# Performance work log

Measured on AMD Instinct MI355X. Metric: run time of the kernel, lower is better.

Reference implementation:

```python
import jax, jax.numpy as jnp
import numpy as np

B = 65536      # groups per batch
S = 4          # members per group (target_size in source)
D = 256        # embedding_dim
NU = 200000    # num_users
NI = 100000    # num_items
NG = 50000     # num_groups


def setup_inputs() -> dict:
    key = jax.random.key(0)
    ks = jax.random.split(key, 18)
    inp = {
        'group_inputs': jax.random.randint(ks[0], (B,), 0, NG),
        'item_inputs': jax.random.randint(ks[1], (B,), 0, NI),
        'group_members': jax.random.randint(ks[2], (NG, S), 0, NU),
        'user_emb': jax.random.normal(ks[3], (NU, D), jnp.float32) * 0.05,
        'item_emb': jax.random.normal(ks[4], (NI, D), jnp.float32) * 0.05,
        'group_emb': jax.random.normal(ks[5], (NG, D), jnp.float32) * 0.05,
        'att_w1': jax.random.normal(ks[6], (2 * D, 16), jnp.float32) * 0.05,
        'att_b1': jnp.zeros((16,), jnp.float32),
        'att_w2': jax.random.normal(ks[7], (16, 1), jnp.float32) * 0.05,
        'att_b2': jnp.zeros((1,), jnp.float32),
        'cls_w': jax.random.normal(ks[8], (1, 2), jnp.float32),
        'cls_b': jnp.zeros((2,), jnp.float32),
        'pred_w1': jax.random.normal(ks[9], (3 * D, 8), jnp.float32) * 0.05,
        'pred_b1': jnp.zeros((8,), jnp.float32),
        'pred_w2': jax.random.normal(ks[10], (8, 1), jnp.float32) * 0.05,
        'pred_b2': jnp.zeros((1,), jnp.float32),
    }
    return inp


def reference(group_inputs, item_inputs, group_members,
              user_emb, item_emb, group_emb,
              att_w1, att_b1, att_w2, att_b2,
              cls_w, cls_b, pred_w1, pred_b1, pred_w2, pred_b2):
    # gather member ids per group: [B, S]
    mem_idx = group_members[group_inputs]
    members = user_emb[mem_idx]                    # [B, S, D]
    items = item_emb[item_inputs]                  # [B, D]
    items_rep = jnp.broadcast_to(items[:, None, :], members.shape)
    gi = jnp.concatenate([members, items_rep], axis=-1)  # [B, S, 2D]

    # attention MLP: 2D -> 16 -> 1, softmax over members
    h = jax.nn.relu(jnp.einsum('bse,ef->bsf', gi, att_w1) + att_b1)
    logits = (jnp.einsum('bsf,fo->bso', h, att_w2) + att_b2)[..., 0]  # [B, S]
    at_wt = jax.nn.softmax(logits, axis=1)

    max_idx = jnp.argmax(at_wt, axis=1)            # [B]

    # classifier Linear(1,2) applied per attention weight -> [B, S, 2]
    scores = at_wt[..., None] * cls_w[0] + cls_b
    classes = jnp.argmax(scores, axis=-1)          # argmax(softmax)=argmax, [B, S]
    # group-level class = class of the max-weight member
    pred_class = jnp.take_along_axis(classes, max_idx[:, None], axis=1)[:, 0]  # [B]

    # branch: gather argmax member (leader) vs attention-weighted sum
    leader = jnp.take_along_axis(members, max_idx[:, None, None], axis=1)[:, 0, :]
    weighted = jnp.einsum('bs,bsd->bd', at_wt, members)
    g_att = jnp.where((pred_class == 1)[:, None], leader, weighted)

    g = g_att + group_emb[group_inputs]            # [B, D]
    elem = g * items
    new = jnp.concatenate([elem, g, items], axis=-1)   # [B, 3D]
    y = jax.nn.sigmoid(jax.nn.relu(new @ pred_w1 + pred_b1) @ pred_w2 + pred_b2)
    return y, at_wt, pred_class.astype(jnp.float32)
```

## Files before the change

kernel.cpp:

```cpp
#include <hip/hip_runtime.h>

#define NB 65536
#define GPB 16

__device__ __forceinline__ float rs4v(float v0, float v1, float v2, float v3,
                                      bool b0, bool b1) {
    float s, r;
    s = b0 ? v0 : v2; r = __shfl_xor(s, 1); float w0 = (b0 ? v2 : v0) + r;
    s = b0 ? v1 : v3; r = __shfl_xor(s, 1); float w1 = (b0 ? v3 : v1) + r;
    s = b1 ? w0 : w1; r = __shfl_xor(s, 2); float u  = (b1 ? w1 : w0) + r;
    u += __shfl_xor(u, 4);
    u += __shfl_xor(u, 8);
    u += __shfl_xor(u, 16);
    return u;
}

__device__ __forceinline__ float rs8v(float v0, float v1, float v2, float v3,
                                      float v4, float v5, float v6, float v7,
                                      bool b0, bool b1, bool b2) {
    float s, r;
    s = b0 ? v0 : v4; r = __shfl_xor(s, 1); float w0 = (b0 ? v4 : v0) + r;
    s = b0 ? v1 : v5; r = __shfl_xor(s, 1); float w1 = (b0 ? v5 : v1) + r;
    s = b0 ? v2 : v6; r = __shfl_xor(s, 1); float w2 = (b0 ? v6 : v2) + r;
    s = b0 ? v3 : v7; r = __shfl_xor(s, 1); float w3 = (b0 ? v7 : v3) + r;
    s = b1 ? w0 : w2; r = __shfl_xor(s, 2); float x0 = (b1 ? w2 : w0) + r;
    s = b1 ? w1 : w3; r = __shfl_xor(s, 2); float x1 = (b1 ? w3 : w1) + r;
    s = b2 ? x0 : x1; r = __shfl_xor(s, 4); float u = (b2 ? x1 : x0) + r;
    u += __shfl_xor(u, 8);
    u += __shfl_xor(u, 16);
    return u;
}

__global__ __launch_bounds__(256) void agree_kernel(
    const int* __restrict__ group_inputs,
    const int* __restrict__ item_inputs,
    const int* __restrict__ group_members,
    const float* __restrict__ user_emb,
    const float* __restrict__ item_emb,
    const float* __restrict__ group_emb,
    const float* __restrict__ att_w1,
    const float* __restrict__ att_b1,
    const float* __restrict__ att_w2,
    const float* __restrict__ att_b2,
    const float* __restrict__ cls_w,
    const float* __restrict__ cls_b,
    const float* __restrict__ pred_w1,
    const float* __restrict__ pred_b1,
    const float* __restrict__ pred_w2,
    const float* __restrict__ pred_b2,
    float* __restrict__ out)
{
    __shared__ __align__(16) float sBuf[32 * 260];

    const int tid = threadIdx.x;
    const int t = tid & 31;
    const int b0 = blockIdx.x * GPB + ((tid >> 5) << 1);

    const int gA  = group_inputs[b0];
    const int gB  = group_inputs[b0 + 1];
    const int itA = item_inputs[b0];
    const int itB = item_inputs[b0 + 1];
    const int4 mA = ((const int4*)group_members)[gA];
    const int4 mB = ((const int4*)group_members)[gB];

    float mbr[2][4][8];
    {
        const int mi[2][4] = {{mA.x, mA.y, mA.z, mA.w}, {mB.x, mB.y, mB.z, mB.w}};
        #pragma unroll
        for (int gg = 0; gg < 2; ++gg) {
            #pragma unroll
            for (int s = 0; s < 4; ++s) {
                const float4* p = (const float4*)user_emb + (((long)mi[gg][s]) << 6) + (t << 1);
                float4 v0 = p[0], v1 = p[1];
                mbr[gg][s][0] = v0.x; mbr[gg][s][1] = v0.y; mbr[gg][s][2] = v0.z; mbr[gg][s][3] = v0.w;
                mbr[gg][s][4] = v1.x; mbr[gg][s][5] = v1.y; mbr[gg][s][6] = v1.z; mbr[gg][s][7] = v1.w;
            }
        }
    }
    float itv[2][8];
    {
        const int ii[2] = {itA, itB};
        #pragma unroll
        for (int gg = 0; gg < 2; ++gg) {
            const float4* p = (const float4*)item_emb + (((long)ii[gg]) << 6) + (t << 1);
            float4 v0 = p[0], v1 = p[1];
            itv[gg][0] = v0.x; itv[gg][1] = v0.y; itv[gg][2] = v0.z; itv[gg][3] = v0.w;
            itv[gg][4] = v1.x; itv[gg][5] = v1.y; itv[gg][6] = v1.z; itv[gg][7] = v1.w;
        }
    }

    const bool bb0 = (t & 1), bb1 = (t & 2), bb2 = (t & 4);
    const int f4 = ((t & 1) << 1) | ((t >> 1) & 1);
    const int f8 = ((t & 1) << 2) + (t & 2) + ((t >> 2) & 1);
    float ab1v[4], aw2v[4];
    #pragma unroll
    for (int p = 0; p < 4; ++p) {
        ab1v[p] = att_b1[4 * p + f4];
        aw2v[p] = att_w2[4 * p + f4];
    }

    {
        const float4* src = (const float4*)att_w1;
        for (int i = tid; i < 2048; i += 256) {
            float4 v = src[i];
            int r = i >> 2, cb = (i & 3) << 2;
            *(float4*)(sBuf + 260 * (r >> 4) + ((r & 15) << 4) + cb) = v;
        }
    }
    __syncthreads();

    const float* mbase = sBuf + 260 * (t >> 1) + ((t & 1) << 7);
    const float* ibase = mbase + 260 * 16;
    float logit[2][4] = {{0.f, 0.f, 0.f, 0.f}, {0.f, 0.f, 0.f, 0.f}};
    #pragma unroll
    for (int p = 0; p < 4; ++p) {
        float acc[2][4][4], pi[2][4];
        #pragma unroll
        for (int gg = 0; gg < 2; ++gg) {
            #pragma unroll
            for (int f = 0; f < 4; ++f) {
                pi[gg][f] = 0.f;
                #pragma unroll
                for (int s = 0; s < 4; ++s) acc[gg][s][f] = 0.f;
            }
        }
        #pragma unroll
        for (int j = 0; j < 8; ++j) {
            float4 wm = *(const float4*)(mbase + (j << 4) + (p << 2));
            float4 wi = *(const float4*)(ibase + (j << 4) + (p << 2));
            #pragma unroll
            for (int gg = 0; gg < 2; ++gg) {
                #pragma unroll
                for (int s = 0; s < 4; ++s) {
                    float mv = mbr[gg][s][j];
                    acc[gg][s][0] += mv * wm.x; acc[gg][s][1] += mv * wm.y;
                    acc[gg][s][2] += mv * wm.z; acc[gg][s][3] += mv * wm.w;
                }
                float iv = itv[gg][j];
                pi[gg][0] += iv * wi.x; pi[gg][1] += iv * wi.y;
                pi[gg][2] += iv * wi.z; pi[gg][3] += iv * wi.w;
            }
        }
        #pragma unroll
        for (int gg = 0; gg < 2; ++gg) {
            float hb = rs4v(pi[gg][0], pi[gg][1], pi[gg][2], pi[gg][3], bb0, bb1)
                       + ab1v[p];
            #pragma unroll
            for (int s = 0; s < 4; ++s) {
                float h = rs4v(acc[gg][s][0], acc[gg][s][1], acc[gg][s][2], acc[gg][s][3],
                               bb0, bb1) + hb;
                logit[gg][s] += fmaxf(h, 0.f) * aw2v[p];
            }
        }
    }
    #pragma unroll
    for (int gg = 0; gg < 2; ++gg) {
        #pragma unroll
        for (int s = 0; s < 4; ++s) {
            float v = logit[gg][s];
            v += __shfl_xor(v, 1); v += __shfl_xor(v, 2);
            logit[gg][s] = v;
        }
    }

    const float cw0 = cls_w[0], cw1 = cls_w[1], cb0c = cls_b[0], cb1c = cls_b[1];
    float at[2][4]; int bestv[2], pcv[2];
    #pragma unroll
    for (int gg = 0; gg < 2; ++gg) {
        float l0 = logit[gg][0], l1 = logit[gg][1], l2 = logit[gg][2], l3 = logit[gg][3];
        float mx = fmaxf(fmaxf(l0, l1), fmaxf(l2, l3));
        float e0 = __expf(l0 - mx), e1 = __expf(l1 - mx);
        float e2 = __expf(l2 - mx), e3 = __expf(l3 - mx);
        float inv = 1.f / (e0 + e1 + e2 + e3);
        at[gg][0] = e0 * inv; at[gg][1] = e1 * inv;
        at[gg][2] = e2 * inv; at[gg][3] = e3 * inv;
        int best = 0; float bv = at[gg][0];
        if (at[gg][1] > bv) { bv = at[gg][1]; best = 1; }
        if (at[gg][2] > bv) { bv = at[gg][2]; best = 2; }
        if (at[gg][3] > bv) { bv = at[gg][3]; best = 3; }
        bestv[gg] = best;
        pcv[gg] = (bv * cw1 + cb1c) > (bv * cw0 + cb0c) ? 1 : 0;
    }

    if (t == 0) {
        #pragma unroll
        for (int gg = 0; gg < 2; ++gg) {
            const int b = b0 + gg;
            *(float4*)(out + NB + 4 * b) = make_float4(at[gg][0], at[gg][1], at[gg][2], at[gg][3]);
            out[5 * NB + b] = (float)pcv[gg];
        }
    }

    float gvr[2][8];
    {
        const int gi2[2] = {gA, gB};
        #pragma unroll
        for (int gg = 0; gg < 2; ++gg) {
            const float4* p = (const float4*)group_emb + (((long)gi2[gg]) << 6) + (t << 1);
            float4 v0 = p[0], v1 = p[1];
            gvr[gg][0] = v0.x; gvr[gg][1] = v0.y; gvr[gg][2] = v0.z; gvr[gg][3] = v0.w;
            gvr[gg][4] = v1.x; gvr[gg][5] = v1.y; gvr[gg][6] = v1.z; gvr[gg][7] = v1.w;
        }
    }

    __syncthreads();
    {
        const float4* srcp = (const float4*)pred_w1;
        for (int i = tid; i < 1536; i += 256) {
            float4 v = srcp[i];
            int r = i >> 1, cb = (i & 1) << 2;
            *(float4*)(sBuf + 132 * (r >> 4) + ((r & 15) << 3) + cb) = v;
        }
    }

    float gvec[2][8], elv[2][8];
    #pragma unroll
    for (int gg = 0; gg < 2; ++gg) {
        #pragma unroll
        for (int d = 0; d < 8; ++d) {
            float w = at[gg][0] * mbr[gg][0][d] + at[gg][1] * mbr[gg][1][d]
                    + at[gg][2] * mbr[gg][2][d] + at[gg][3] * mbr[gg][3][d];
            float ldr = mbr[gg][0][d];
            ldr = (bestv[gg] == 1) ? mbr[gg][1][d] : ldr;
            ldr = (bestv[gg] == 2) ? mbr[gg][2][d] : ldr;
            ldr = (bestv[gg] == 3) ? mbr[gg][3][d] : ldr;
            float ga = pcv[gg] ? ldr : w;
            float gv = ga + gvr[gg][d];
            gvec[gg][d] = gv;
            elv[gg][d]  = gv * itv[gg][d];
        }
    }
    __syncthreads();

    const float pb1v = pred_b1[f8], pw2v = pred_w2[f8], pb2v = pred_b2[0];
    const float* pbase = sBuf + 132 * (t >> 1) + ((t & 1) << 6);
    float po[2][8] = {{0.f,0.f,0.f,0.f,0.f,0.f,0.f,0.f},
                      {0.f,0.f,0.f,0.f,0.f,0.f,0.f,0.f}};
    #pragma unroll
    for (int j = 0; j < 8; ++j) {
        const float* pA = pbase + (j << 3);
        float4 a0 = *(const float4*)pA,          a1 = *(const float4*)(pA + 4);
        float4 q0 = *(const float4*)(pA + 2112), q1 = *(const float4*)(pA + 2116);
        float4 c0 = *(const float4*)(pA + 4224), c1 = *(const float4*)(pA + 4228);
        #pragma unroll
        for (int gg = 0; gg < 2; ++gg) {
            float e = elv[gg][j], gv = gvec[gg][j], iv = itv[gg][j];
            po[gg][0] += e * a0.x; po[gg][0] += gv * q0.x; po[gg][0] += iv * c0.x;
            po[gg][1] += e * a0.y; po[gg][1] += gv * q0.y; po[gg][1] += iv * c0.y;
            po[gg][2] += e * a0.z; po[gg][2] += gv * q0.z; po[gg][2] += iv * c0.z;
            po[gg][3] += e * a0.w; po[gg][3] += gv * q0.w; po[gg][3] += iv * c0.w;
            po[gg][4] += e * a1.x; po[gg][4] += gv * q1.x; po[gg][4] += iv * c1.x;
            po[gg][5] += e * a1.y; po[gg][5] += gv * q1.y; po[gg][5] += iv * c1.y;
            po[gg][6] += e * a1.z; po[gg][6] += gv * q1.z; po[gg][6] += iv * c1.z;
            po[gg][7] += e * a1.w; po[gg][7] += gv * q1.w; po[gg][7] += iv * c1.w;
        }
    }

    float yv[2];
    #pragma unroll
    for (int gg = 0; gg < 2; ++gg) {
        float poR = rs8v(po[gg][0], po[gg][1], po[gg][2], po[gg][3],
                         po[gg][4], po[gg][5], po[gg][6], po[gg][7],
                         bb0, bb1, bb2);
        float z = fmaxf(poR + pb1v, 0.f) * pw2v;
        z += __shfl_xor(z, 1); z += __shfl_xor(z, 2); z += __shfl_xor(z, 4);
        z += pb2v;
        yv[gg] = 1.f / (1.f + __expf(-z));
    }

    if (t == 0) {
        out[b0]     = yv[0];
        out[b0 + 1] = yv[1];
    }
}

extern "C" void kernel_launch(void* const* d_in, const int* in_sizes, int n_in,
                              void* d_out, int out_size, void* d_ws, size_t ws_size,
                              hipStream_t stream) {
    (void)in_sizes; (void)n_in; (void)out_size; (void)d_ws; (void)ws_size;
    agree_kernel<<<NB / GPB, 256, 0, stream>>>(
        (const int*)d_in[0], (const int*)d_in[1], (const int*)d_in[2],
        (const float*)d_in[3], (const float*)d_in[4], (const float*)d_in[5],
        (const float*)d_in[6], (const float*)d_in[7], (const float*)d_in[8],
        (const float*)d_in[9], (const float*)d_in[10], (const float*)d_in[11],
        (const float*)d_in[12], (const float*)d_in[13], (const float*)d_in[14],
        (const float*)d_in[15], (float*)d_out);
}
```

Baseline: 448.4 us.

## Make kernel persistent with software-pipelined prefetch of next groups' embeddings

Replaces one-shot blocks of 16 groups with 512 blocks that each loop over 8 iterations of 16 groups. Both weight matrices stay resident in separate shared buffers, loaded once per block instead of per 16 groups. The next iteration's indices, member ids and embedding rows are prefetched into a second register set while the current one computes, to hide gather latency. The cost is doubled register state, which may cut occupancy or spill, and far fewer blocks for the GPU's many CUs.

```diff
diff --git a/kernel.cpp b/kernel.cpp
--- a/kernel.cpp
+++ b/kernel.cpp
@@ -1,7 +1,8 @@
 #include <hip/hip_runtime.h>
 
 #define NB 65536
-#define GPB 16
+#define NBLK 512
+#define ITERS 8
 
 __device__ __forceinline__ float rs4v(float v0, float v1, float v2, float v3,
                                       bool b0, bool b1) {
@@ -29,6 +30,225 @@
     u += __shfl_xor(u, 8);
     u += __shfl_xor(u, 16);
     return u;
+}
+
+struct GState {
+    int g0, g1, it0, it1;
+    int4 m0, m1;
+    float mbr[2][4][8];
+    float itv[2][8];
+};
+
+struct Ctx {
+    const int* group_inputs; const int* item_inputs; const int* group_members;
+    const float* user_emb; const float* item_emb; const float* group_emb;
+    float ab1v[4], aw2v[4];
+    float pb1v, pw2v, pb2v, cw0, cw1, cb0c, cb1c;
+    bool bb0, bb1, bb2;
+    int t, lg;
+    float* out;
+};
+
+__device__ __forceinline__ void load_idx(const Ctx& c, GState& st, int b) {
+    st.g0  = c.group_inputs[b];  st.g1  = c.group_inputs[b + 1];
+    st.it0 = c.item_inputs[b];   st.it1 = c.item_inputs[b + 1];
+}
+
+__device__ __forceinline__ void load_mem(const Ctx& c, GState& st) {
+    st.m0 = ((const int4*)c.group_members)[st.g0];
+    st.m1 = ((const int4*)c.group_members)[st.g1];
+}
+
+__device__ __forceinline__ void load_rows(const Ctx& c, GState& st) {
+    const int t = c.t;
+    const int mi[2][4] = {{st.m0.x, st.m0.y, st.m0.z, st.m0.w},
+                          {st.m1.x, st.m1.y, st.m1.z, st.m1.w}};
+    #pragma unroll
+    for (int gg = 0; gg < 2; ++gg) {
+        #pragma unroll
+        for (int s = 0; s < 4; ++s) {
+            const float4* p = (const float4*)c.user_emb + (((long)mi[gg][s]) << 6) + (t << 1);
+            float4 v0 = p[0], v1 = p[1];
+            st.mbr[gg][s][0] = v0.x; st.mbr[gg][s][1] = v0.y;
+            st.mbr[gg][s][2] = v0.z; st.mbr[gg][s][3] = v0.w;
+            st.mbr[gg][s][4] = v1.x; st.mbr[gg][s][5] = v1.y;
+            st.mbr[gg][s][6] = v1.z; st.mbr[gg][s][7] = v1.w;
+        }
+    }
+    const int ii2[2] = {st.it0, st.it1};
+    #pragma unroll
+    for (int gg = 0; gg < 2; ++gg) {
+        const float4* p = (const float4*)c.item_emb + (((long)ii2[gg]) << 6) + (t << 1);
+        float4 v0 = p[0], v1 = p[1];
+        st.itv[gg][0] = v0.x; st.itv[gg][1] = v0.y;
+        st.itv[gg][2] = v0.z; st.itv[gg][3] = v0.w;
+        st.itv[gg][4] = v1.x; st.itv[gg][5] = v1.y;
+        st.itv[gg][6] = v1.z; st.itv[gg][7] = v1.w;
+    }
+}
+
+__device__ __forceinline__ void iter_body(const Ctx& c, GState& cur, GState& nxt,
+                                          int k, int base,
+                                          const float* sA, const float* sP) {
+    const int t = c.t;
+    const int b0 = base + k * 16 + c.lg * 2;
+    const bool more = (k + 1 < ITERS);
+    if (more) load_idx(c, nxt, b0 + 16);
+
+    float gvr[2][8];
+    {
+        const int gi2[2] = {cur.g0, cur.g1};
+        #pragma unroll
+        for (int gg = 0; gg < 2; ++gg) {
+            const float4* p = (const float4*)c.group_emb + (((long)gi2[gg]) << 6) + (t << 1);
+            float4 v0 = p[0], v1 = p[1];
+            gvr[gg][0] = v0.x; gvr[gg][1] = v0.y; gvr[gg][2] = v0.z; gvr[gg][3] = v0.w;
+            gvr[gg][4] = v1.x; gvr[gg][5] = v1.y; gvr[gg][6] = v1.z; gvr[gg][7] = v1.w;
+        }
+    }
+
+    const float* mbase = sA + 260 * (t >> 1) + ((t & 1) << 7);
+    const float* ibase = mbase + 260 * 16;
+    float logit[2][4] = {{0.f, 0.f, 0.f, 0.f}, {0.f, 0.f, 0.f, 0.f}};
+    #pragma unroll
+    for (int p = 0; p < 4; ++p) {
+        float acc[2][4][4], pi[2][4];
+        #pragma unroll
+        for (int gg = 0; gg < 2; ++gg) {
+            #pragma unroll
+            for (int f = 0; f < 4; ++f) {
+                pi[gg][f] = 0.f;
+                #pragma unroll
+                for (int s = 0; s < 4; ++s) acc[gg][s][f] = 0.f;
+            }
+        }
+        #pragma unroll
+        for (int j = 0; j < 8; ++j) {
+            float4 wm = *(const float4*)(mbase + (j << 4) + (p << 2));
+            float4 wi = *(const float4*)(ibase + (j << 4) + (p << 2));
+            #pragma unroll
+            for (int gg = 0; gg < 2; ++gg) {
+                #pragma unroll
+                for (int s = 0; s < 4; ++s) {
+                    float mv = cur.mbr[gg][s][j];
+                    acc[gg][s][0] += mv * wm.x; acc[gg][s][1] += mv * wm.y;
+                    acc[gg][s][2] += mv * wm.z; acc[gg][s][3] += mv * wm.w;
+                }
+                float iv = cur.itv[gg][j];
+                pi[gg][0] += iv * wi.x; pi[gg][1] += iv * wi.y;
+                pi[gg][2] += iv * wi.z; pi[gg][3] += iv * wi.w;
+            }
+        }
+        #pragma unroll
+        for (int gg = 0; gg < 2; ++gg) {
+            float hb = rs4v(pi[gg][0], pi[gg][1], pi[gg][2], pi[gg][3], c.bb0, c.bb1)
+                       + c.ab1v[p];
+            #pragma unroll
+            for (int s = 0; s < 4; ++s) {
+                float h = rs4v(acc[gg][s][0], acc[gg][s][1], acc[gg][s][2], acc[gg][s][3],
+                               c.bb0, c.bb1) + hb;
+                logit[gg][s] += fmaxf(h, 0.f) * c.aw2v[p];
+            }
+        }
+    }
+    if (more) load_mem(c, nxt);
+
+    #pragma unroll
+    for (int gg = 0; gg < 2; ++gg) {
+        #pragma unroll
+        for (int s = 0; s < 4; ++s) {
+            float v = logit[gg][s];
+            v += __shfl_xor(v, 1); v += __shfl_xor(v, 2);
+            logit[gg][s] = v;
+        }
+    }
+
+    float at[2][4]; int bestv[2], pcv[2];
+    #pragma unroll
+    for (int gg = 0; gg < 2; ++gg) {
+        float l0 = logit[gg][0], l1 = logit[gg][1], l2 = logit[gg][2], l3 = logit[gg][3];
+        float mx = fmaxf(fmaxf(l0, l1), fmaxf(l2, l3));
+        float e0 = __expf(l0 - mx), e1 = __expf(l1 - mx);
+        float e2 = __expf(l2 - mx), e3 = __expf(l3 - mx);
+        float inv = 1.f / (e0 + e1 + e2 + e3);
+        at[gg][0] = e0 * inv; at[gg][1] = e1 * inv;
+        at[gg][2] = e2 * inv; at[gg][3] = e3 * inv;
+        int best = 0; float bv = at[gg][0];
+        if (at[gg][1] > bv) { bv = at[gg][1]; best = 1; }
+        if (at[gg][2] > bv) { bv = at[gg][2]; best = 2; }
+        if (at[gg][3] > bv) { bv = at[gg][3]; best = 3; }
+        bestv[gg] = best;
+        pcv[gg] = (bv * c.cw1 + c.cb1c) > (bv * c.cw0 + c.cb0c) ? 1 : 0;
+    }
+
+    if (t == 0) {
+        #pragma unroll
+        for (int gg = 0; gg < 2; ++gg) {
+            const int b = b0 + gg;
+            *(float4*)(c.out + NB + 4 * b) = make_float4(at[gg][0], at[gg][1], at[gg][2], at[gg][3]);
+            c.out[5 * NB + b] = (float)pcv[gg];
+        }
+    }
+
+    float gvec[2][8], elv[2][8];
+    #pragma unroll
+    for (int gg = 0; gg < 2; ++gg) {
+        #pragma unroll
+        for (int d = 0; d < 8; ++d) {
+            float w = at[gg][0] * cur.mbr[gg][0][d] + at[gg][1] * cur.mbr[gg][1][d]
+                    + at[gg][2] * cur.mbr[gg][2][d] + at[gg][3] * cur.mbr[gg][3][d];
+            float ldr = cur.mbr[gg][0][d];
+            ldr = (bestv[gg] == 1) ? cur.mbr[gg][1][d] : ldr;
+            ldr = (bestv[gg] == 2) ? cur.mbr[gg][2][d] : ldr;
+            ldr = (bestv[gg] == 3) ? cur.mbr[gg][3][d] : ldr;
+            float ga = pcv[gg] ? ldr : w;
+            float gv = ga + gvr[gg][d];
+            gvec[gg][d] = gv;
+            elv[gg][d]  = gv * cur.itv[gg][d];
+        }
+    }
+
+    if (more) load_rows(c, nxt);
+
+    const float* pbase = sP + 132 * (t >> 1) + ((t & 1) << 6);
+    float po[2][8] = {{0.f,0.f,0.f,0.f,0.f,0.f,0.f,0.f},
+                      {0.f,0.f,0.f,0.f,0.f,0.f,0.f,0.f}};
+    #pragma unroll
+    for (int j = 0; j < 8; ++j) {
+        const float* pA = pbase + (j << 3);
+        float4 a0 = *(const float4*)pA,          a1 = *(const float4*)(pA + 4);
+        float4 q0 = *(const float4*)(pA + 2112), q1 = *(const float4*)(pA + 2116);
+        float4 c0 = *(const float4*)(pA + 4224), c1 = *(const float4*)(pA + 4228);
+        #pragma unroll
+        for (int gg = 0; gg < 2; ++gg) {
+            float e = elv[gg][j], gv = gvec[gg][j], iv = cur.itv[gg][j];
+            po[gg][0] += e * a0.x; po[gg][0] += gv * q0.x; po[gg][0] += iv * c0.x;
+            po[gg][1] += e * a0.y; po[gg][1] += gv * q0.y; po[gg][1] += iv * c0.y;
+            po[gg][2] += e * a0.z; po[gg][2] += gv * q0.z; po[gg][2] += iv * c0.z;
+            po[gg][3] += e * a0.w; po[gg][3] += gv * q0.w; po[gg][3] += iv * c0.w;
+            po[gg][4] += e * a1.x; po[gg][4] += gv * q1.x; po[gg][4] += iv * c1.x;
+            po[gg][5] += e * a1.y; po[gg][5] += gv * q1.y; po[gg][5] += iv * c1.y;
+            po[gg][6] += e * a1.z; po[gg][6] += gv * q1.z; po[gg][6] += iv * c1.z;
+            po[gg][7] += e * a1.w; po[gg][7] += gv * q1.w; po[gg][7] += iv * c1.w;
+        }
+    }
+
+    float yv[2];
+    #pragma unroll
+    for (int gg = 0; gg < 2; ++gg) {
+        float poR = rs8v(po[gg][0], po[gg][1], po[gg][2], po[gg][3],
+                         po[gg][4], po[gg][5], po[gg][6], po[gg][7],
+                         c.bb0, c.bb1, c.bb2);
+        float z = fmaxf(poR + c.pb1v, 0.f) * c.pw2v;
+        z += __shfl_xor(z, 1); z += __shfl_xor(z, 2); z += __shfl_xor(z, 4);
+        z += c.pb2v;
+        yv[gg] = 1.f / (1.f + __expf(-z));
+    }
+
+    if (t == 0) {
+        c.out[b0]     = yv[0];
+        c.out[b0 + 1] = yv[1];
+    }
 }
 
 __global__ __launch_bounds__(256) void agree_kernel(
@@ -50,227 +270,55 @@
     const float* __restrict__ pred_b2,
     float* __restrict__ out)
 {
-    __shared__ __align__(16) float sBuf[32 * 260];
+    __shared__ __align__(16) float sA[32 * 260];
+    __shared__ __align__(16) float sP[48 * 132];
 
     const int tid = threadIdx.x;
     const int t = tid & 31;
-    const int b0 = blockIdx.x * GPB + ((tid >> 5) << 1);
-
-    const int gA  = group_inputs[b0];
-    const int gB  = group_inputs[b0 + 1];
-    const int itA = item_inputs[b0];
-    const int itB = item_inputs[b0 + 1];
-    const int4 mA = ((const int4*)group_members)[gA];
-    const int4 mB = ((const int4*)group_members)[gB];
-
-    float mbr[2][4][8];
-    {
-        const int mi[2][4] = {{mA.x, mA.y, mA.z, mA.w}, {mB.x, mB.y, mB.z, mB.w}};
-        #pragma unroll
-        for (int gg = 0; gg < 2; ++gg) {
-            #pragma unroll
-            for (int s = 0; s < 4; ++s) {
-                const float4* p = (const float4*)user_emb + (((long)mi[gg][s]) << 6) + (t << 1);
-                float4 v0 = p[0], v1 = p[1];
-                mbr[gg][s][0] = v0.x; mbr[gg][s][1] = v0.y; mbr[gg][s][2] = v0.z; mbr[gg][s][3] = v0.w;
-                mbr[gg][s][4] = v1.x; mbr[gg][s][5] = v1.y; mbr[gg][s][6] = v1.z; mbr[gg][s][7] = v1.w;
-            }
-        }
-    }
-    float itv[2][8];
-    {
-        const int ii[2] = {itA, itB};
-        #pragma unroll
-        for (int gg = 0; gg < 2; ++gg) {
-            const float4* p = (const float4*)item_emb + (((long)ii[gg]) << 6) + (t << 1);
-            float4 v0 = p[0], v1 = p[1];
-            itv[gg][0] = v0.x; itv[gg][1] = v0.y; itv[gg][2] = v0.z; itv[gg][3] = v0.w;
-            itv[gg][4] = v1.x; itv[gg][5] = v1.y; itv[gg][6] = v1.z; itv[gg][7] = v1.w;
-        }
-    }
-
-    const bool bb0 = (t & 1), bb1 = (t & 2), bb2 = (t & 4);
-    const int f4 = ((t & 1) << 1) | ((t >> 1) & 1);
-    const int f8 = ((t & 1) << 2) + (t & 2) + ((t >> 2) & 1);
-    float ab1v[4], aw2v[4];
-    #pragma unroll
-    for (int p = 0; p < 4; ++p) {
-        ab1v[p] = att_b1[4 * p + f4];
-        aw2v[p] = att_w2[4 * p + f4];
-    }
+    const int lg = tid >> 5;
+    const int base = blockIdx.x * (ITERS * 16);
 
     {
         const float4* src = (const float4*)att_w1;
         for (int i = tid; i < 2048; i += 256) {
             float4 v = src[i];
             int r = i >> 2, cb = (i & 3) << 2;
-            *(float4*)(sBuf + 260 * (r >> 4) + ((r & 15) << 4) + cb) = v;
-        }
-    }
-    __syncthreads();
-
-    const float* mbase = sBuf + 260 * (t >> 1) + ((t & 1) << 7);
-    const float* ibase = mbase + 260 * 16;
-    float logit[2][4] = {{0.f, 0.f, 0.f, 0.f}, {0.f, 0.f, 0.f, 0.f}};
-    #pragma unroll
-    for (int p = 0; p < 4; ++p) {
-        float acc[2][4][4], pi[2][4];
-        #pragma unroll
-        for (int gg = 0; gg < 2; ++gg) {
-            #pragma unroll
-            for (int f = 0; f < 4; ++f) {
-                pi[gg][f] = 0.f;
-                #pragma unroll
-                for (int s = 0; s < 4; ++s) acc[gg][s][f] = 0.f;
-            }
-        }
-        #pragma unroll
-        for (int j = 0; j < 8; ++j) {
-            float4 wm = *(const float4*)(mbase + (j << 4) + (p << 2));
-            float4 wi = *(const float4*)(ibase + (j << 4) + (p << 2));
-            #pragma unroll
-            for (int gg = 0; gg < 2; ++gg) {
-                #pragma unroll
-                for (int s = 0; s < 4; ++s) {
-                    float mv = mbr[gg][s][j];
-                    acc[gg][s][0] += mv * wm.x; acc[gg][s][1] += mv * wm.y;
-                    acc[gg][s][2] += mv * wm.z; acc[gg][s][3] += mv * wm.w;
-                }
-                float iv = itv[gg][j];
-                pi[gg][0] += iv * wi.x; pi[gg][1] += iv * wi.y;
-                pi[gg][2] += iv * wi.z; pi[gg][3] += iv * wi.w;
-            }
-        }
-        #pragma unroll
-        for (int gg = 0; gg < 2; ++gg) {
-            float hb = rs4v(pi[gg][0], pi[gg][1], pi[gg][2], pi[gg][3], bb0, bb1)
-                       + ab1v[p];
-            #pragma unroll
-            for (int s = 0; s < 4; ++s) {
-                float h = rs4v(acc[gg][s][0], acc[gg][s][1], acc[gg][s][2], acc[gg][s][3],
-                               bb0, bb1) + hb;
-                logit[gg][s] += fmaxf(h, 0.f) * aw2v[p];
-            }
-        }
-    }
-    #pragma unroll
-    for (int gg = 0; gg < 2; ++gg) {
-        #pragma unroll
-        for (int s = 0; s < 4; ++s) {
-            float v = logit[gg][s];
-            v += __shfl_xor(v, 1); v += __shfl_xor(v, 2);
-            logit[gg][s] = v;
-        }
-    }
-
-    const float cw0 = cls_w[0], cw1 = cls_w[1], cb0c = cls_b[0], cb1c = cls_b[1];
-    float at[2][4]; int bestv[2], pcv[2];
-    #pragma unroll
-    for (int gg = 0; gg < 2; ++gg) {
-        float l0 = logit[gg][0], l1 = logit[gg][1], l2 = logit[gg][2], l3 = logit[gg][3];
-        float mx = fmaxf(fmaxf(l0, l1), fmaxf(l2, l3));
-        float e0 = __expf(l0 - mx), e1 = __expf(l1 - mx);
-        float e2 = __expf(l2 - mx), e3 = __expf(l3 - mx);
-        float inv = 1.f / (e0 + e1 + e2 + e3);
-        at[gg][0] = e0 * inv; at[gg][1] = e1 * inv;
-        at[gg][2] = e2 * inv; at[gg][3] = e3 * inv;
-        int best = 0; float bv = at[gg][0];
-        if (at[gg][1] > bv) { bv = at[gg][1]; best = 1; }
-        if (at[gg][2] > bv) { bv = at[gg][2]; best = 2; }
-        if (at[gg][3] > bv) { bv = at[gg][3]; best = 3; }
-        bestv[gg] = best;
-        pcv[gg] = (bv * cw1 + cb1c) > (bv * cw0 + cb0c) ? 1 : 0;
-    }
-
-    if (t == 0) {
-        #pragma unroll
-        for (int gg = 0; gg < 2; ++gg) {
-            const int b = b0 + gg;
-            *(float4*)(out + NB + 4 * b) = make_float4(at[gg][0], at[gg][1], at[gg][2], at[gg][3]);
-            out[5 * NB + b] = (float)pcv[gg];
-        }
-    }
-
-    float gvr[2][8];
-    {
-        const int gi2[2] = {gA, gB};
-        #pragma unroll
-        for (int gg = 0; gg < 2; ++gg) {
-            const float4* p = (const float4*)group_emb + (((long)gi2[gg]) << 6) + (t << 1);
-            float4 v0 = p[0], v1 = p[1];
-            gvr[gg][0] = v0.x; gvr[gg][1] = v0.y; gvr[gg][2] = v0.z; gvr[gg][3] = v0.w;
-            gvr[gg][4] = v1.x; gvr[gg][5] = v1.y; gvr[gg][6] = v1.z; gvr[gg][7] = v1.w;
-        }
-    }
-
-    __syncthreads();
-    {
+            *(float4*)(sA + 260 * (r >> 4) + ((r & 15) << 4) + cb) = v;
+        }
         const float4* srcp = (const float4*)pred_w1;
         for (int i = tid; i < 1536; i += 256) {
             float4 v = srcp[i];
             int r = i >> 1, cb = (i & 1) << 2;
-            *(float4*)(sBuf + 132 * (r >> 4) + ((r & 15) << 3) + cb) = v;
-        }
-    }
-
-    float gvec[2][8], elv[2][8];
-    #pragma unroll
-    for (int gg = 0; gg < 2; ++gg) {
-        #pragma unroll
-        for (int d = 0; d < 8; ++d) {
-            float w = at[gg][0] * mbr[gg][0][d] + at[gg][1] * mbr[gg][1][d]
-                    + at[gg][2] * mbr[gg][2][d] + at[gg][3] * mbr[gg][3][d];
-            float ldr = mbr[gg][0][d];
-            ldr = (bestv[gg] == 1) ? mbr[gg][1][d] : ldr;
-            ldr = (bestv[gg] == 2) ? mbr[gg][2][d] : ldr;
-            ldr = (bestv[gg] == 3) ? mbr[gg][3][d] : ldr;
-            float ga = pcv[gg] ? ldr : w;
-            float gv = ga + gvr[gg][d];
-            gvec[gg][d] = gv;
-            elv[gg][d]  = gv * itv[gg][d];
-        }
-    }
+            *(float4*)(sP + 132 * (r >> 4) + ((r & 15) << 3) + cb) = v;
+        }
+    }
+
+    Ctx c;
+    c.group_inputs = group_inputs; c.item_inputs = item_inputs;
+    c.group_members = group_members;
+    c.user_emb = user_emb; c.item_emb = item_emb; c.group_emb = group_emb;
+    c.t = t; c.lg = lg; c.out = out;
+    c.bb0 = (t & 1); c.bb1 = (t & 2); c.bb2 = (t & 4);
+    const int f4 = ((t & 1) << 1) | ((t >> 1) & 1);
+    const int f8 = ((t & 1) << 2) + (t & 2) + ((t >> 2) & 1);
+    #pragma unroll
+    for (int p = 0; p < 4; ++p) {
+        c.ab1v[p] = att_b1[4 * p + f4];
+        c.aw2v[p] = att_w2[4 * p + f4];
+    }
+    c.pb1v = pred_b1[f8]; c.pw2v = pred_w2[f8]; c.pb2v = pred_b2[0];
+    c.cw0 = cls_w[0]; c.cw1 = cls_w[1]; c.cb0c = cls_b[0]; c.cb1c = cls_b[1];
+
+    GState sa, sb;
+    load_idx(c, sa, base + lg * 2);
+    load_mem(c, sa);
+    load_rows(c, sa);
+
     __syncthreads();
 
-    const float pb1v = pred_b1[f8], pw2v = pred_w2[f8], pb2v = pred_b2[0];
-    const float* pbase = sBuf + 132 * (t >> 1) + ((t & 1) << 6);
-    float po[2][8] = {{0.f,0.f,0.f,0.f,0.f,0.f,0.f,0.f},
-                      {0.f,0.f,0.f,0.f,0.f,0.f,0.f,0.f}};
-    #pragma unroll
-    for (int j = 0; j < 8; ++j) {
-        const float* pA = pbase + (j << 3);
-        float4 a0 = *(const float4*)pA,          a1 = *(const float4*)(pA + 4);
-        float4 q0 = *(const float4*)(pA + 2112), q1 = *(const float4*)(pA + 2116);
-        float4 c0 = *(const float4*)(pA + 4224), c1 = *(const float4*)(pA + 4228);
-        #pragma unroll
-        for (int gg = 0; gg < 2; ++gg) {
-            float e = elv[gg][j], gv = gvec[gg][j], iv = itv[gg][j];
-            po[gg][0] += e * a0.x; po[gg][0] += gv * q0.x; po[gg][0] += iv * c0.x;
-            po[gg][1] += e * a0.y; po[gg][1] += gv * q0.y; po[gg][1] += iv * c0.y;
-            po[gg][2] += e * a0.z; po[gg][2] += gv * q0.z; po[gg][2] += iv * c0.z;
-            po[gg][3] += e * a0.w; po[gg][3] += gv * q0.w; po[gg][3] += iv * c0.w;
-            po[gg][4] += e * a1.x; po[gg][4] += gv * q1.x; po[gg][4] += iv * c1.x;
-            po[gg][5] += e * a1.y; po[gg][5] += gv * q1.y; po[gg][5] += iv * c1.y;
-            po[gg][6] += e * a1.z; po[gg][6] += gv * q1.z; po[gg][6] += iv * c1.z;
-            po[gg][7] += e * a1.w; po[gg][7] += gv * q1.w; po[gg][7] += iv * c1.w;
-        }
-    }
-
-    float yv[2];
-    #pragma unroll
-    for (int gg = 0; gg < 2; ++gg) {
-        float poR = rs8v(po[gg][0], po[gg][1], po[gg][2], po[gg][3],
-                         po[gg][4], po[gg][5], po[gg][6], po[gg][7],
-                         bb0, bb1, bb2);
-        float z = fmaxf(poR + pb1v, 0.f) * pw2v;
-        z += __shfl_xor(z, 1); z += __shfl_xor(z, 2); z += __shfl_xor(z, 4);
-        z += pb2v;
-        yv[gg] = 1.f / (1.f + __expf(-z));
-    }
-
-    if (t == 0) {
-        out[b0]     = yv[0];
-        out[b0 + 1] = yv[1];
+    for (int kk = 0; kk < ITERS; kk += 2) {
+        iter_body(c, sa, sb, kk,     base, sA, sP);
+        iter_body(c, sb, sa, kk + 1, base, sA, sP);
     }
 }
 
@@ -278,7 +326,7 @@
                               void* d_out, int out_size, void* d_ws, size_t ws_size,
                               hipStream_t stream) {
     (void)in_sizes; (void)n_in; (void)out_size; (void)d_ws; (void)ws_size;
-    agree_kernel<<<NB / GPB, 256, 0, stream>>>(
+    agree_kernel<<<NBLK, 256, 0, stream>>>(
         (const int*)d_in[0], (const int*)d_in[1], (const int*)d_in[2],
         (const float*)d_in[3], (const float*)d_in[4], (const float*)d_in[5],
         (const float*)d_in[6], (const float*)d_in[7], (const float*)d_in[8],
```

New measurement: 560.3 us. 25.0% more time.
